# Optimization experiments

Measured on AMD Instinct MI355X. Metric: run time of the kernel, lower is better.

The kernel has to match this reference:

```python
import jax, jax.numpy as jnp
import numpy as np
import math

B, C, H, W = 8, 64, 128, 128
OUT, HEADS, K, S = 32, 8, 3, 2
DH = C // HEADS
PAD = (K - 1) // 2
EPS = 1e-5


def _unfold(t, k):
    # t: [B, C, H, W] -> per-pixel kxk windows [B*H*W, k*k, C] (torch.nn.Unfold layout: channel-major)
    b, c, h, w = t.shape
    pat = jax.lax.conv_general_dilated_patches(t, (k, k), (1, 1), [(PAD, PAD), (PAD, PAD)])  # [B, C*k*k, H, W]
    pat = pat.reshape(b, c, k * k, h * w)          # [B, C, k^2, HW]
    return jnp.transpose(pat, (0, 3, 2, 1)).reshape(b * h * w, k * k, c)


def setup_inputs() -> dict:
    key = jax.random.key(0)
    ks = jax.random.split(key, 18)
    def n(k, shape, sc=0.05):
        return jax.random.normal(k, shape, jnp.float32) * sc
    return {
        "x": jax.random.normal(ks[0], (B, C, H, W), jnp.float32),
        "up_query": jax.random.normal(ks[1], (1, S * S, C), jnp.float32),  # learned up-sampling queries
        "Wk": n(ks[2], (C, C)), "bk": n(ks[3], (C,), 0.02),   # to_k 1x1 conv
        "Wv": n(ks[4], (C, C)), "bv": n(ks[5], (C,), 0.02),   # to_v 1x1 conv
        "Wq": n(ks[6], (C, C)), "bq": n(ks[7], (C,), 0.02),   # MHA q proj
        "Wka": n(ks[8], (C, C)), "bka": n(ks[9], (C,), 0.02), # MHA k proj
        "Wva": n(ks[10], (C, C)), "bva": n(ks[11], (C,), 0.02),  # MHA v proj
        "Wo": n(ks[12], (C, OUT)), "bo": n(ks[13], (OUT,), 0.02),  # MHA output proj (project_dim=out_dim)
        "rel_pos": n(ks[14], (1, HEADS, S * S, K * K), 1.0),  # learned relative positional bias
        "ln_g": jnp.ones((OUT,), jnp.float32),
        "ln_b": jnp.zeros((OUT,), jnp.float32),
    }


def reference(x, up_query, Wk, bk, Wv, bv, Wq, bq, Wka, bka, Wva, bva, Wo, bo, rel_pos, ln_g, ln_b):
    b, c, h, w = x.shape
    # pre_norm = Identity (post_norm=True). pe_k = Identity (pos_embedding=None).
    kf = jnp.einsum('bchw,cd->bdhw', x, Wk) + bk[None, :, None, None]
    vf = jnp.einsum('bchw,cd->bdhw', x, Wv) + bv[None, :, None, None]
    # aux_zeros branch: to_k(pe(zeros)) == conv bias -> adds bk to every window position
    xk = _unfold(kf, K) + bk[None, None, :]            # [N, k^2, C]
    xv = _unfold(vf, K)                                # [N, k^2, C]
    n = xk.shape[0]
    xq = jnp.broadcast_to(up_query, (n, S * S, c))     # [N, s^2, C]
    # multi-head attention with relative positional bias on logits
    qh = (xq @ Wq + bq).reshape(n, S * S, HEADS, DH)
    kh = (xk @ Wka + bka).reshape(n, K * K, HEADS, DH)
    vh = (xv @ Wva + bva).reshape(n, K * K, HEADS, DH)
    logits = jnp.einsum('nqhd,nkhd->nhqk', qh, kh) / math.sqrt(DH) + rel_pos  # [N, h, s^2, k^2]
    attn = jax.nn.softmax(logits, axis=-1)
    out = jnp.einsum('nhqk,nkhd->nqhd', attn, vh).reshape(n, S * S, c)
    out = out @ Wo + bo                                # [N, s^2, OUT]
    # post LayerNorm over out_dim
    mu = jnp.mean(out, axis=-1, keepdims=True)
    var = jnp.mean(jnp.square(out - mu), axis=-1, keepdims=True)
    out = (out - mu) / jnp.sqrt(var + EPS) * ln_g + ln_b
    # pixel-shuffle style reshape to [B, OUT, H*s, W*s]
    out = out.reshape(b, h, w, S, S, OUT)
    out = jnp.transpose(out, (0, 5, 1, 3, 2, 4)).reshape(b, OUT, h * S, w * S)
    return out
```

## Files before the change

### kernel.cpp

```cpp
#include <hip/hip_runtime.h>

#define HW    16384
#define WIDTH 128
#define LOG2E    1.4426950408889634f
#define RS_LOG2E 0.5101464200926166f

#define WFB_DWORDS 4992
#define WOT_DWORDS 1024
#define REL_OFF    (WFB_DWORDS + WOT_DWORDS)

typedef short bshort8 __attribute__((ext_vector_type(8)));
typedef _Float16 half8 __attribute__((ext_vector_type(8)));
typedef float f32x4   __attribute__((ext_vector_type(4)));
typedef unsigned u32x4 __attribute__((ext_vector_type(4)));
typedef unsigned u32x2 __attribute__((ext_vector_type(2)));

static __device__ inline unsigned short f2bf(float f) {
    unsigned u = __builtin_bit_cast(unsigned, f);
    unsigned r = u + 0x7fff + ((u >> 16) & 1);
    return (unsigned short)(r >> 16);
}
static __device__ inline unsigned cvtpk(float lo, float hi) {
    unsigned d;
    asm("v_cvt_pk_bf16_f32 %0, %1, %2" : "=v"(d) : "v"(lo), "v"(hi));
    return d;
}
static __device__ inline unsigned pkrtz(float lo, float hi) {
    return __builtin_bit_cast(unsigned, __builtin_amdgcn_cvt_pkrtz(lo, hi));
}
static __device__ inline unsigned pkfma16_lo(unsigned o, unsigned a, unsigned v) {
    asm("v_pk_fma_f16 %0, %1, %2, %0 op_sel:[0,0,0] op_sel_hi:[0,1,1]"
        : "+v"(o) : "v"(a), "v"(v));
    return o;
}
static __device__ inline unsigned pkfma16_hi(unsigned o, unsigned a, unsigned v) {
    asm("v_pk_fma_f16 %0, %1, %2, %0 op_sel:[1,0,0] op_sel_hi:[1,1,1]"
        : "+v"(o) : "v"(a), "v"(v));
    return o;
}
static __device__ inline unsigned pkmul16_lo(unsigned a, unsigned r) {
    unsigned d;
    asm("v_pk_mul_f16 %0, %1, %2 op_sel:[0,0] op_sel_hi:[0,1]"
        : "=v"(d) : "v"(r), "v"(a));
    return d;
}
static __device__ inline unsigned pkmul16_hi(unsigned a, unsigned r) {
    unsigned d;
    asm("v_pk_mul_f16 %0, %1, %2 op_sel:[1,0] op_sel_hi:[1,1]"
        : "=v"(d) : "v"(r), "v"(a));
    return d;
}

__global__ __launch_bounds__(256) void k0_fuse(
    const float* __restrict__ up_query,
    const float* __restrict__ Wk, const float* __restrict__ bk,
    const float* __restrict__ Wv, const float* __restrict__ bv,
    const float* __restrict__ Wq, const float* __restrict__ bq,
    const float* __restrict__ Wka, const float* __restrict__ bka,
    const float* __restrict__ Wva, const float* __restrict__ bva,
    const float* __restrict__ Wo, const float* __restrict__ rel_pos,
    float* __restrict__ ws)
{
    __shared__ float qcS[4][64];
    __shared__ float WkT[64][65];
    __shared__ float WvT[64][65];
    __shared__ float colS[12][64];
    __shared__ float bred[12][8];
    __shared__ float pred[12][8];

    const int tid = threadIdx.x;
    const int bj  = blockIdx.x;
    const int j0  = bj * 12;

    {
        int q = tid >> 6, f = tid & 63;
        float a = bq[f];
        for (int c = 0; c < 64; ++c) a = fmaf(up_query[q*64+c], Wq[c*64+f], a);
        qcS[q][f] = a;
    }
    for (int i = tid; i < 4096; i += 256) {
        int c = i >> 6, e = i & 63;
        WkT[e][c] = Wk[i];
        WvT[e][c] = Wv[i];
    }
    __syncthreads();

    for (int i = tid; i < 768; i += 256) {
        int jl = i >> 6, e = i & 63;
        int j = j0 + jl;
        float v;
        if (j < 32) {
            int h = j >> 2, qq = j & 3;
            float s = 0.f;
            #pragma unroll
            for (int d = 0; d < 8; ++d)
                s = fmaf(Wka[e*64 + h*8 + d], qcS[qq][h*8 + d], s);
            v = s * RS_LOG2E;
        } else {
            v = Wva[e*64 + (j - 32)];
        }
        colS[jl][e] = v;
    }
    if (tid < 96) {
        int jl = tid >> 3, d = tid & 7;
        int j = j0 + jl;
        if (j < 32) {
            int h = j >> 2, qq = j & 3;
            int fi = h*8 + d;
            float bW = 0.f;
            for (int e = 0; e < 64; ++e) bW = fmaf(bk[e], Wka[e*64 + fi], bW);
            float qv = qcS[qq][fi];
            bred[jl][d] = (2.f*bW + bka[fi]) * qv;
            pred[jl][d] = bW * qv;
        } else {
            float s = 0.f;
            for (int e = d*8; e < d*8 + 8; ++e)
                s = fmaf(bv[e], Wva[e*64 + (j - 32)], s);
            bred[jl][d] = s;
            pred[jl][d] = 0.f;
        }
    }
    __syncthreads();

    unsigned* wsd = (unsigned*)ws;
    for (int i = tid; i < 384; i += 256) {
        int cp = i & 31, jl = i >> 5;
        int j = j0 + jl;
        const float (*MT)[65] = (j < 32) ? WkT : WvT;
        float o0 = 0.f, o1 = 0.f;
        for (int e = 0; e < 64; ++e) {
            float cv = colS[jl][e];
            o0 = fmaf(MT[e][2*cp],     cv, o0);
            o1 = fmaf(MT[e][2*cp + 1], cv, o1);
        }
        wsd[j*52 + cp] = (unsigned)f2bf(o0) | ((unsigned)f2bf(o1) << 16);
    }
    for (int i = tid; i < 240; i += 256) {
        int jl = i / 20, kd = 32 + (i % 20);
        int j = j0 + jl;
        unsigned val = 0u;
        if (kd == 32) {
            float sv = 0.f, sp = 0.f;
            #pragma unroll
            for (int d = 0; d < 8; ++d) { sv += bred[jl][d]; sp += pred[jl][d]; }
            float bf_, pd_;
            if (j < 32) { bf_ = sv * RS_LOG2E; pd_ = (sv - sp) * RS_LOG2E; }
            else        { bf_ = sv + bva[j-32]; pd_ = bva[j-32]; }
            val = (unsigned)f2bf(bf_) | ((unsigned)f2bf(pd_) << 16);
        }
        wsd[j*52 + kd] = val;
    }
    if (bj == 7) {
        for (int i = tid; i < WOT_DWORDS; i += 256) {
            int col = i >> 5, kp = i & 31;
            wsd[WFB_DWORDS + i] = pkrtz(Wo[(2*kp)*32 + col], Wo[(2*kp + 1)*32 + col]);
        }
        for (int i = tid; i < 288; i += 256)
            ws[REL_OFF + i] = rel_pos[i] * LOG2E;
    }
}

__global__ __launch_bounds__(256, 5) void k2_attn(
    const float* __restrict__ x, const float* __restrict__ ws,
    const float* __restrict__ bo,
    const float* __restrict__ ln_g, const float* __restrict__ ln_b,
    float* __restrict__ out)
{
    __shared__ __align__(16) char smem[32768];

    const int tid = threadIdx.x;

    const int flat = blockIdx.x;
    const int wg   = (flat & 7) * 256 + (flat >> 3);
    const int tx = wg & 15;
    const int ty = (wg >> 4) & 15;
    const int b  = wg >> 8;

    #pragma unroll
    for (int it = 0; it < 6; ++it) {
        int i = tid + it*256;
        int p = i & 127, kq = i >> 7;
        if (p < 112) {
            u32x4 pack = {0u, 0u, 0u, 0u};
            if (p < 100) {
                int py = p / 10, px = p - py*10;
                int gy = ty*8 - 1 + py, gx = tx*8 - 1 + px;
                bool valid = ((unsigned)gy < 128u) && ((unsigned)gx < 128u);
                if (kq < 8) {
                    if (valid) {
                        const float* xp = x + ((size_t)b*64 + kq*8)*HW + gy*WIDTH + gx;
                        #pragma unroll
                        for (int e = 0; e < 4; ++e)
                            pack[e] = cvtpk(xp[(size_t)(2*e)*HW], xp[(size_t)(2*e+1)*HW]);
                    }
                } else if (kq == 8) {
                    pack[0] = valid ? 0x00003f80u : 0x3f800000u;
                }
            }
            *(u32x4*)(smem + p*256 + (((unsigned)(kq*16)) ^ (((unsigned)(p & 7)) << 4))) = pack;
        }
    }
    __syncthreads();

    const int lane = tid & 63;
    const int wv   = tid >> 6;
    const int frow = lane & 15;
    const int kseg = lane >> 4;

    const unsigned short* wfs = (const unsigned short*)ws;
    f32x4 accs[11];
    #pragma unroll
    for (int tt = 0; tt < 11; ++tt) {
        int t = wv + 4*tt;
        if (t < 42) {
            int mt = t / 6, nt = t - mt*6;
            int prow = mt*16 + frow;
            const unsigned psw = ((unsigned)(prow & 7)) << 4;
            const unsigned short* wrow = wfs + (nt*16 + frow)*104 + kseg*8;
            f32x4 acc = {0.f, 0.f, 0.f, 0.f};
            #pragma unroll
            for (int kk = 0; kk < 3; ++kk) {
                bshort8 wf = *(const bshort8*)(wrow + kk*32);
                bshort8 xa = *(const bshort8*)(smem + prow*256
                                 + (((unsigned)(kseg*16 + kk*64)) ^ psw));
                acc = __builtin_amdgcn_mfma_f32_16x16x32_bf16(wf, xa, acc, 0, 0, 0);
            }
            accs[tt] = acc;
        }
    }
    __syncthreads();

    unsigned short* Lh = (unsigned short*)smem;
    unsigned short* Vh = (unsigned short*)(smem + 8192);
    #pragma unroll
    for (int tt = 0; tt < 11; ++tt) {
        int t = wv + 4*tt;
        if (t < 42) {
            int mt = t / 6, nt = t - mt*6;
            int p = mt*16 + frow;
            if (p < 100) {
                u32x2 dd = { pkrtz(accs[tt][0], accs[tt][1]),
                             pkrtz(accs[tt][2], accs[tt][3]) };
                if (nt < 2) *(u32x2*)(Lh + p*36 + nt*16 + kseg*4) = dd;
                else        *(u32x2*)(Vh + p*72 + (nt-2)*16 + kseg*4) = dd;
            }
        }
    }
    __syncthreads();

    const int dpy = lane >> 3, dpx = lane & 7;
    const int pbase = dpy*10 + dpx;
    const float* relw = ws + REL_OFF;

    unsigned od[32];
    #pragma unroll
    for (int hh = 0; hh < 2; ++hh) {
        const int h = wv*2 + hh;
        unsigned apk[2][9];
        float rinv[4];
        #pragma unroll
        for (int qp = 0; qp < 2; ++qp) {
            const int hq0 = h*4 + qp*2;
            float l0[9], l1[9];
            #pragma unroll
            for (int n = 0; n < 9; ++n) {
                const int off = (n/3)*10 + (n%3);
                l0[n] = exp2f((float)*(const _Float16*)(Lh + (pbase+off)*36 + hq0)
                              + relw[hq0*9 + n]);
                l1[n] = exp2f((float)*(const _Float16*)(Lh + (pbase+off)*36 + hq0 + 1)
                              + relw[(hq0+1)*9 + n]);
            }
            float s0 = ((l0[0]+l0[1]) + (l0[2]+l0[3]))
                     + ((l0[4]+l0[5]) + (l0[6]+l0[7])) + l0[8];
            float s1 = ((l1[0]+l1[1]) + (l1[2]+l1[3]))
                     + ((l1[4]+l1[5]) + (l1[6]+l1[7])) + l1[8];
            rinv[qp*2]     = __builtin_amdgcn_rcpf(s0);
            rinv[qp*2 + 1] = __builtin_amdgcn_rcpf(s1);
            #pragma unroll
            for (int n = 0; n < 9; ++n) apk[qp][n] = pkrtz(l0[n], l1[n]);
        }
        unsigned o16[4][4] = {{0u,0u,0u,0u},{0u,0u,0u,0u},{0u,0u,0u,0u},{0u,0u,0u,0u}};
        #pragma unroll
        for (int n = 0; n < 9; ++n) {
            const int off = (n/3)*10 + (n%3);
            const u32x4 v4 = *(const u32x4*)(Vh + (pbase + off)*72 + h*8);
            #pragma unroll
            for (int j = 0; j < 4; ++j) {
                o16[0][j] = pkfma16_lo(o16[0][j], apk[0][n], v4[j]);
                o16[1][j] = pkfma16_hi(o16[1][j], apk[0][n], v4[j]);
                o16[2][j] = pkfma16_lo(o16[2][j], apk[1][n], v4[j]);
                o16[3][j] = pkfma16_hi(o16[3][j], apk[1][n], v4[j]);
            }
        }
        const unsigned r01 = pkrtz(rinv[0], rinv[1]);
        const unsigned r23 = pkrtz(rinv[2], rinv[3]);
        #pragma unroll
        for (int j = 0; j < 4; ++j) {
            od[(0*2 + hh)*4 + j] = pkmul16_lo(o16[0][j], r01);
            od[(1*2 + hh)*4 + j] = pkmul16_hi(o16[1][j], r01);
            od[(2*2 + hh)*4 + j] = pkmul16_lo(o16[2][j], r23);
            od[(3*2 + hh)*4 + j] = pkmul16_hi(o16[3][j], r23);
        }
    }
    __syncthreads();

    {
        const unsigned sw = ((unsigned)(lane & 7)) << 4;
        #pragma unroll
        for (int q = 0; q < 4; ++q) {
            const int row = lane*4 + q;
            #pragma unroll
            for (int hh = 0; hh < 2; ++hh) {
                u32x4 w4 = { od[(q*2+hh)*4+0], od[(q*2+hh)*4+1],
                             od[(q*2+hh)*4+2], od[(q*2+hh)*4+3] };
                *(u32x4*)(smem + row*128 + (((unsigned)(wv*32 + hh*16)) ^ sw)) = w4;
            }
        }
    }
    __syncthreads();

    const unsigned short* wotu = (const unsigned short*)ws + WFB_DWORDS*2;
    half8 av[4][2];
    #pragma unroll
    for (int mt = 0; mt < 4; ++mt) {
        const int row = wv*64 + mt*16 + frow;
        const unsigned sw = (((unsigned)(row >> 2)) & 7u) << 4;
        #pragma unroll
        for (int ks = 0; ks < 2; ++ks)
            av[mt][ks] = __builtin_bit_cast(half8,
                *(const u32x4*)(smem + row*128 + (((unsigned)(kseg*16 + ks*64)) ^ sw)));
    }
    half8 bv_[2][2];
    #pragma unroll
    for (int nt = 0; nt < 2; ++nt) {
        const int col = nt*16 + frow;
        #pragma unroll
        for (int ks = 0; ks < 2; ++ks)
            bv_[nt][ks] = __builtin_bit_cast(half8,
                *(const u32x4*)(wotu + col*64 + kseg*8 + ks*32));
    }
    f32x4 cacc[4][2];
    #pragma unroll
    for (int mt = 0; mt < 4; ++mt)
        #pragma unroll
        for (int nt = 0; nt < 2; ++nt)
            cacc[mt][nt] = (f32x4){0.f, 0.f, 0.f, 0.f};
    #pragma unroll
    for (int ks = 0; ks < 2; ++ks)
        #pragma unroll
        for (int mt = 0; mt < 4; ++mt)
            #pragma unroll
            for (int nt = 0; nt < 2; ++nt)
                cacc[mt][nt] = __builtin_amdgcn_mfma_f32_16x16x32_f16(
                    av[mt][ks], bv_[nt][ks], cacc[mt][nt], 0, 0, 0);

    #pragma unroll
    for (int mt = 0; mt < 4; ++mt)
        #pragma unroll
        for (int nt = 0; nt < 2; ++nt)
            #pragma unroll
            for (int r = 0; r < 4; ++r) {
                const int row = wv*64 + mt*16 + kseg*4 + r;
                const int col = nt*16 + frow;
                *(float*)(smem + row*128
                    + (((unsigned)(col*4)) ^ ((((unsigned)(row >> 2)) & 7u) << 4)))
                    = cacc[mt][nt][r];
            }
    asm volatile("s_waitcnt lgkmcnt(0)" ::: "memory");

    float cv[32];
    {
        const unsigned sw = (((unsigned)(tid >> 2)) & 7u) << 4;
        #pragma unroll
        for (int j = 0; j < 8; ++j) {
            const f32x4 c4 = *(const f32x4*)(smem + tid*128 + (((unsigned)(j*16)) ^ sw));
            cv[j*4+0] = c4[0]; cv[j*4+1] = c4[1]; cv[j*4+2] = c4[2]; cv[j*4+3] = c4[3];
        }
    }
    float mu = 0.f;
    #pragma unroll
    for (int oc = 0; oc < 32; ++oc) { cv[oc] += bo[oc]; mu += cv[oc]; }
    mu *= (1.f/32.f);
    float var = 0.f;
    #pragma unroll
    for (int oc = 0; oc < 32; ++oc) { float d = cv[oc] - mu; var += d*d; }
    var *= (1.f/32.f);
    const float rstd = rsqrtf(var + 1e-5f);

    const int q   = tid & 3;
    const int pix = tid >> 2;
    const int gy = ty*8 + (pix >> 3), gx = tx*8 + (pix & 7);
    const int Y = gy*2 + (q >> 1), X = gx*2 + (q & 1);
    float* op = out + (((size_t)b*32)*256 + Y)*256 + X;
    #pragma unroll
    for (int oc = 0; oc < 32; ++oc) {
        float v = (cv[oc] - mu) * rstd * ln_g[oc] + ln_b[oc];
        op[(size_t)oc * 65536] = v;
    }
}

extern "C" void kernel_launch(void* const* d_in, const int* in_sizes, int n_in,
                              void* d_out, int out_size, void* d_ws, size_t ws_size,
                              hipStream_t stream)
{
    const float* x        = (const float*)d_in[0];
    const float* up_query = (const float*)d_in[1];
    const float* Wk  = (const float*)d_in[2];
    const float* bk  = (const float*)d_in[3];
    const float* Wv  = (const float*)d_in[4];
    const float* bv  = (const float*)d_in[5];
    const float* Wq  = (const float*)d_in[6];
    const float* bq  = (const float*)d_in[7];
    const float* Wka = (const float*)d_in[8];
    const float* bka = (const float*)d_in[9];
    const float* Wva = (const float*)d_in[10];
    const float* bva = (const float*)d_in[11];
    const float* Wo  = (const float*)d_in[12];
    const float* bo  = (const float*)d_in[13];
    const float* rel_pos = (const float*)d_in[14];
    const float* ln_g = (const float*)d_in[15];
    const float* ln_b = (const float*)d_in[16];

    float* ws  = (float*)d_ws;
    float* out = (float*)d_out;

    if (ws_size < (size_t)(REL_OFF + 288) * 4) return;

    k0_fuse<<<8, 256, 0, stream>>>(up_query, Wk, bk, Wv, bv, Wq, bq,
                                   Wka, bka, Wva, bva, Wo, rel_pos, ws);
    k2_attn<<<2048, 256, 0, stream>>>(x, ws, bo, ln_g, ln_b, out);
}
```

Baseline: 63.88 us.

## Reuse A fragments across N tiles, compact staging loop, vectorize logit loads

The projection GEMM now gives each wave two full M-tiles, loading the three activation fragments once and reusing them across all six N-tiles instead of reloading per tile. The input staging loop indexes 1200 packed items directly with a magic-number divide, cutting the sixth iteration and the padded slots. The softmax stage reads four head logits with one 8-byte LDS load and keeps running sums rather than scalar loads and tree sums. Work per wave becomes less even, since wave 3 gets a single M-tile while the others get two, and the extra live accumulators may raise register pressure under the occupancy bound.

```diff
diff --git a/kernel.cpp b/kernel.cpp
--- a/kernel.cpp
+++ b/kernel.cpp
@@ -27,6 +27,12 @@
 }
 static __device__ inline unsigned pkrtz(float lo, float hi) {
     return __builtin_bit_cast(unsigned, __builtin_amdgcn_cvt_pkrtz(lo, hi));
+}
+static __device__ inline float lo16f(unsigned u) {
+    return (float)__builtin_bit_cast(_Float16, (unsigned short)(u & 0xffffu));
+}
+static __device__ inline float hi16f(unsigned u) {
+    return (float)__builtin_bit_cast(_Float16, (unsigned short)(u >> 16));
 }
 static __device__ inline unsigned pkfma16_lo(unsigned o, unsigned a, unsigned v) {
     asm("v_pk_fma_f16 %0, %1, %2, %0 op_sel:[0,0,0] op_sel_hi:[0,1,1]"
@@ -177,25 +183,24 @@
     const int b  = wg >> 8;
 
     #pragma unroll
-    for (int it = 0; it < 6; ++it) {
+    for (int it = 0; it < 5; ++it) {
         int i = tid + it*256;
-        int p = i & 127, kq = i >> 7;
-        if (p < 112) {
+        if (i < 1200) {
+            int kq = (int)(((unsigned)i * 5243u) >> 19);
+            int p  = i - kq*100;
+            int py = p / 10, px = p - py*10;
+            int gy = ty*8 - 1 + py, gx = tx*8 - 1 + px;
+            bool valid = ((unsigned)gy < 128u) && ((unsigned)gx < 128u);
             u32x4 pack = {0u, 0u, 0u, 0u};
-            if (p < 100) {
-                int py = p / 10, px = p - py*10;
-                int gy = ty*8 - 1 + py, gx = tx*8 - 1 + px;
-                bool valid = ((unsigned)gy < 128u) && ((unsigned)gx < 128u);
-                if (kq < 8) {
-                    if (valid) {
-                        const float* xp = x + ((size_t)b*64 + kq*8)*HW + gy*WIDTH + gx;
-                        #pragma unroll
-                        for (int e = 0; e < 4; ++e)
-                            pack[e] = cvtpk(xp[(size_t)(2*e)*HW], xp[(size_t)(2*e+1)*HW]);
-                    }
-                } else if (kq == 8) {
-                    pack[0] = valid ? 0x00003f80u : 0x3f800000u;
+            if (kq < 8) {
+                if (valid) {
+                    const float* xp = x + ((size_t)b*64 + kq*8)*HW + gy*WIDTH + gx;
+                    #pragma unroll
+                    for (int e = 0; e < 4; ++e)
+                        pack[e] = cvtpk(xp[(size_t)(2*e)*HW], xp[(size_t)(2*e+1)*HW]);
                 }
+            } else if (kq == 8) {
+                pack[0] = valid ? 0x00003f80u : 0x3f800000u;
             }
             *(u32x4*)(smem + p*256 + (((unsigned)(kq*16)) ^ (((unsigned)(p & 7)) << 4))) = pack;
         }
@@ -208,24 +213,25 @@
     const int kseg = lane >> 4;
 
     const unsigned short* wfs = (const unsigned short*)ws;
-    f32x4 accs[11];
-    #pragma unroll
-    for (int tt = 0; tt < 11; ++tt) {
-        int t = wv + 4*tt;
-        if (t < 42) {
-            int mt = t / 6, nt = t - mt*6;
-            int prow = mt*16 + frow;
+    f32x4 accs[12];
+    #pragma unroll
+    for (int mi = 0; mi < 2; ++mi) {
+        const int mt = wv*2 + mi;
+        if (mt < 7) {
+            const int prow = mt*16 + frow;
             const unsigned psw = ((unsigned)(prow & 7)) << 4;
-            const unsigned short* wrow = wfs + (nt*16 + frow)*104 + kseg*8;
-            f32x4 acc = {0.f, 0.f, 0.f, 0.f};
-            #pragma unroll
-            for (int kk = 0; kk < 3; ++kk) {
-                bshort8 wf = *(const bshort8*)(wrow + kk*32);
-                bshort8 xa = *(const bshort8*)(smem + prow*256
-                                 + (((unsigned)(kseg*16 + kk*64)) ^ psw));
-                acc = __builtin_amdgcn_mfma_f32_16x16x32_bf16(wf, xa, acc, 0, 0, 0);
-            }
-            accs[tt] = acc;
+            bshort8 xa0 = *(const bshort8*)(smem + prow*256 + (((unsigned)(kseg*16))       ^ psw));
+            bshort8 xa1 = *(const bshort8*)(smem + prow*256 + (((unsigned)(kseg*16 + 64))  ^ psw));
+            bshort8 xa2 = *(const bshort8*)(smem + prow*256 + (((unsigned)(kseg*16 + 128)) ^ psw));
+            #pragma unroll
+            for (int nt = 0; nt < 6; ++nt) {
+                const unsigned short* wrow = wfs + (nt*16 + frow)*104 + kseg*8;
+                f32x4 acc = {0.f, 0.f, 0.f, 0.f};
+                acc = __builtin_amdgcn_mfma_f32_16x16x32_bf16(*(const bshort8*)(wrow),      xa0, acc, 0, 0, 0);
+                acc = __builtin_amdgcn_mfma_f32_16x16x32_bf16(*(const bshort8*)(wrow + 32), xa1, acc, 0, 0, 0);
+                acc = __builtin_amdgcn_mfma_f32_16x16x32_bf16(*(const bshort8*)(wrow + 64), xa2, acc, 0, 0, 0);
+                accs[mi*6 + nt] = acc;
+            }
         }
     }
     __syncthreads();
@@ -233,16 +239,18 @@
     unsigned short* Lh = (unsigned short*)smem;
     unsigned short* Vh = (unsigned short*)(smem + 8192);
     #pragma unroll
-    for (int tt = 0; tt < 11; ++tt) {
-        int t = wv + 4*tt;
-        if (t < 42) {
-            int mt = t / 6, nt = t - mt*6;
-            int p = mt*16 + frow;
+    for (int mi = 0; mi < 2; ++mi) {
+        const int mt = wv*2 + mi;
+        if (mt < 7) {
+            const int p = mt*16 + frow;
             if (p < 100) {
-                u32x2 dd = { pkrtz(accs[tt][0], accs[tt][1]),
-                             pkrtz(accs[tt][2], accs[tt][3]) };
-                if (nt < 2) *(u32x2*)(Lh + p*36 + nt*16 + kseg*4) = dd;
-                else        *(u32x2*)(Vh + p*72 + (nt-2)*16 + kseg*4) = dd;
+                #pragma unroll
+                for (int nt = 0; nt < 6; ++nt) {
+                    const f32x4 acc = accs[mi*6 + nt];
+                    u32x2 dd = { pkrtz(acc[0], acc[1]), pkrtz(acc[2], acc[3]) };
+                    if (nt < 2) *(u32x2*)(Lh + p*36 + nt*16 + kseg*4) = dd;
+                    else        *(u32x2*)(Vh + p*72 + (nt-2)*16 + kseg*4) = dd;
+                }
             }
         }
     }
@@ -257,28 +265,23 @@
     for (int hh = 0; hh < 2; ++hh) {
         const int h = wv*2 + hh;
         unsigned apk[2][9];
-        float rinv[4];
-        #pragma unroll
-        for (int qp = 0; qp < 2; ++qp) {
-            const int hq0 = h*4 + qp*2;
-            float l0[9], l1[9];
-            #pragma unroll
-            for (int n = 0; n < 9; ++n) {
-                const int off = (n/3)*10 + (n%3);
-                l0[n] = exp2f((float)*(const _Float16*)(Lh + (pbase+off)*36 + hq0)
-                              + relw[hq0*9 + n]);
-                l1[n] = exp2f((float)*(const _Float16*)(Lh + (pbase+off)*36 + hq0 + 1)
-                              + relw[(hq0+1)*9 + n]);
-            }
-            float s0 = ((l0[0]+l0[1]) + (l0[2]+l0[3]))
-                     + ((l0[4]+l0[5]) + (l0[6]+l0[7])) + l0[8];
-            float s1 = ((l1[0]+l1[1]) + (l1[2]+l1[3]))
-                     + ((l1[4]+l1[5]) + (l1[6]+l1[7])) + l1[8];
-            rinv[qp*2]     = __builtin_amdgcn_rcpf(s0);
-            rinv[qp*2 + 1] = __builtin_amdgcn_rcpf(s1);
-            #pragma unroll
-            for (int n = 0; n < 9; ++n) apk[qp][n] = pkrtz(l0[n], l1[n]);
-        }
+        float s0 = 0.f, s1 = 0.f, s2 = 0.f, s3 = 0.f;
+        const float* rp = relw + h*36;
+        #pragma unroll
+        for (int n = 0; n < 9; ++n) {
+            const int off = (n/3)*10 + (n%3);
+            const u32x2 L4 = *(const u32x2*)(Lh + (pbase + off)*36 + h*4);
+            float e0 = exp2f(lo16f(L4[0]) + rp[n]);
+            float e1 = exp2f(hi16f(L4[0]) + rp[9 + n]);
+            float e2 = exp2f(lo16f(L4[1]) + rp[18 + n]);
+            float e3 = exp2f(hi16f(L4[1]) + rp[27 + n]);
+            s0 += e0; s1 += e1; s2 += e2; s3 += e3;
+            apk[0][n] = pkrtz(e0, e1);
+            apk[1][n] = pkrtz(e2, e3);
+        }
+        const unsigned r01 = pkrtz(__builtin_amdgcn_rcpf(s0), __builtin_amdgcn_rcpf(s1));
+        const unsigned r23 = pkrtz(__builtin_amdgcn_rcpf(s2), __builtin_amdgcn_rcpf(s3));
+
         unsigned o16[4][4] = {{0u,0u,0u,0u},{0u,0u,0u,0u},{0u,0u,0u,0u},{0u,0u,0u,0u}};
         #pragma unroll
         for (int n = 0; n < 9; ++n) {
@@ -292,8 +295,6 @@
                 o16[3][j] = pkfma16_hi(o16[3][j], apk[1][n], v4[j]);
             }
         }
-        const unsigned r01 = pkrtz(rinv[0], rinv[1]);
-        const unsigned r23 = pkrtz(rinv[2], rinv[3]);
         #pragma unroll
         for (int j = 0; j < 4; ++j) {
             od[(0*2 + hh)*4 + j] = pkmul16_lo(o16[0][j], r01);
```

After: 62.34 us. 1.02x faster.
